# Kernel optimization log

Measured on AMD Instinct MI355X. Metric: run time of the kernel, lower is better.

## Reference

```python
import jax, jax.numpy as jnp
import numpy as np

H = 8
D = 64  # head_dim = node_dim // num_heads = 512 // 8
NODE = 512
EPS = 1e-5


def setup_inputs() -> dict:
    key = jax.random.key(0)
    ks = jax.random.split(key, 8)
    S, IN = 4096, 1024
    return {
        "protT5_emb": jax.random.normal(ks[0], (S, IN), jnp.float32),
        "contact_matrix": jax.random.uniform(ks[1], (S, S), jnp.float32),
        "Wq": jax.random.normal(ks[2], (NODE, IN), jnp.float32) * 0.02,
        "bq": jnp.zeros((NODE,), jnp.float32),
        "Wk": jax.random.normal(ks[3], (NODE, IN), jnp.float32) * 0.02,
        "bk": jnp.zeros((NODE,), jnp.float32),
        "Wv": jax.random.normal(ks[4], (NODE, IN), jnp.float32) * 0.02,
        "bv": jnp.zeros((NODE,), jnp.float32),
        "Wc": jnp.ones((1, H, 1, 1), jnp.float32),
        "Wo": jax.random.normal(ks[5], (NODE, NODE), jnp.float32) * 0.02,
        "bo": jnp.zeros((NODE,), jnp.float32),
        "gamma": jnp.ones((NODE,), jnp.float32),
        "beta": jnp.zeros((NODE,), jnp.float32),
    }


def reference(protT5_emb, contact_matrix, Wq, bq, Wk, bk, Wv, bv, Wc, Wo, bo, gamma, beta):
    S = protT5_emb.shape[0]
    # QKV projections -> [H, S, D]
    Q = (protT5_emb @ Wq.T + bq).reshape(S, H, D).transpose(1, 0, 2)
    K = (protT5_emb @ Wk.T + bk).reshape(S, H, D).transpose(1, 0, 2)
    V = (protT5_emb @ Wv.T + bv).reshape(S, H, D).transpose(1, 0, 2)
    # raw scores [H, S, S]
    attn_raw = jnp.einsum('hsd,htd->hst', Q, K) / jnp.sqrt(jnp.float32(D))
    # multiplicative contact mask, per-head learnable scale
    contact_mask = contact_matrix[None, :, :] * Wc.reshape(H, 1, 1)
    attn_weight = jax.nn.softmax(attn_raw * contact_mask, axis=-1)
    attn_output = jnp.einsum('hst,htd->hsd', attn_weight, V)  # [H, S, D]
    # FAITHFUL to torch: transpose(0,1).view(S,-1) on [1,H,S,D] flattens in
    # (head, seq, dim) order -> scrambled [S, H*D] reshape, not head concat.
    attn_output = attn_output.reshape(S, H * D)
    aug = attn_output @ Wo.T + bo
    x = aug + protT5_emb[:, :NODE]
    mu = jnp.mean(x, axis=-1, keepdims=True)
    var = jnp.mean((x - mu) ** 2, axis=-1, keepdims=True)
    return (x - mu) * jax.lax.rsqrt(var + EPS) * gamma + beta
```

## Files before the change

kernel.cpp:

```cpp
#include <hip/hip_runtime.h>
#include <stdint.h>

#define SEQ 4096
#define INDIM 1024
#define NODEDIM 512
#define NH 8
#define HD 64
#define LSTR 72

typedef __bf16 bf16x8 __attribute__((ext_vector_type(8)));
typedef float f32x4 __attribute__((ext_vector_type(4)));

__device__ __forceinline__ unsigned short f2bf(float f) {
    union { float f; uint32_t u; } v; v.f = f;
    uint32_t u = v.u;
    uint32_t r = (u + 0x7fffu + ((u >> 16) & 1u)) >> 16;
    return (unsigned short)r;
}

__device__ __forceinline__ float fast_exp2(float x) {
    float r;
    asm volatile("v_exp_f32 %0, %1" : "=v"(r) : "v"(x));
    return r;
}

__global__ __launch_bounds__(256) void cvt_all(const float* __restrict__ emb,
                                               const float* __restrict__ Wq,
                                               const float* __restrict__ Wk,
                                               const float* __restrict__ Wv,
                                               const float* __restrict__ Wo,
                                               unsigned short* __restrict__ demb,
                                               unsigned short* __restrict__ dwqkv,
                                               unsigned short* __restrict__ dwo) {
    int b = blockIdx.x;
    const float* src;
    unsigned short* dst;
    int off;
    if (b < 4096)      { src = emb; dst = demb;            off = b; }
    else if (b < 4608) { src = Wq;  dst = dwqkv;           off = b - 4096; }
    else if (b < 5120) { src = Wk;  dst = dwqkv + 524288;  off = b - 4608; }
    else if (b < 5632) { src = Wv;  dst = dwqkv + 1048576; off = b - 5120; }
    else               { src = Wo;  dst = dwo;             off = b - 5632; }
    int i = (off * 256 + threadIdx.x) * 4;
    float4 v = *(const float4*)(src + i);
    ushort4 o;
    o.x = f2bf(v.x); o.y = f2bf(v.y); o.z = f2bf(v.z); o.w = f2bf(v.w);
    *(ushort4*)(dst + i) = o;
}

__global__ __launch_bounds__(256) void qkv_gemm(const unsigned short* __restrict__ A,
                                                const unsigned short* __restrict__ B,
                                                const float* __restrict__ bq,
                                                const float* __restrict__ bk,
                                                const float* __restrict__ bv,
                                                unsigned short* __restrict__ Qo,
                                                unsigned short* __restrict__ Ko,
                                                unsigned short* __restrict__ VTo) {
    __shared__ unsigned short As[128 * 32];
    __shared__ unsigned short Bs[128 * 32];
    __shared__ unsigned short Ts[128 * 40];
    const int tid = threadIdx.x;
    const int lane = tid & 63, wave = tid >> 6;
    const int wm = wave >> 1, wn = wave & 1;
    const int quad = lane >> 4, l16 = lane & 15;
    const int m0 = blockIdx.x * 128;
    const int n0 = blockIdx.y * 128;

    f32x4 acc[4][4] = {};

    for (int k0 = 0; k0 < INDIM; k0 += 32) {
        __syncthreads();
        for (int i = 0; i < 2; ++i) {
            int c = tid + 256 * i;
            int row = c >> 2, qq = c & 3;
            *(bf16x8*)&As[row * 32 + qq * 8] =
                *(const bf16x8*)(A + (size_t)(m0 + row) * INDIM + k0 + qq * 8);
            *(bf16x8*)&Bs[row * 32 + qq * 8] =
                *(const bf16x8*)(B + (size_t)(n0 + row) * INDIM + k0 + qq * 8);
        }
        __syncthreads();
        bf16x8 af[4], bf[4];
        for (int mi = 0; mi < 4; ++mi)
            af[mi] = *(const bf16x8*)&As[(wm * 64 + mi * 16 + l16) * 32 + quad * 8];
        for (int ni = 0; ni < 4; ++ni)
            bf[ni] = *(const bf16x8*)&Bs[(wn * 64 + ni * 16 + l16) * 32 + quad * 8];
        for (int mi = 0; mi < 4; ++mi)
            for (int ni = 0; ni < 4; ++ni)
                acc[mi][ni] = __builtin_amdgcn_mfma_f32_16x16x32_bf16(af[mi], bf[ni], acc[mi][ni], 0, 0, 0);
    }

    if (blockIdx.y < 8) {
        unsigned short* outp = (blockIdx.y < 4) ? Qo : Ko;
        const float* biasp = (blockIdx.y < 4) ? bq : bk;
        for (int mi = 0; mi < 4; ++mi)
            for (int ni = 0; ni < 4; ++ni)
                for (int r = 0; r < 4; ++r) {
                    int s = m0 + wm * 64 + mi * 16 + quad * 4 + r;
                    int n = n0 + wn * 64 + ni * 16 + l16;
                    int h = (n >> 6) & 7;
                    int dd = n & 63;
                    float v = acc[mi][ni][r] + biasp[n & 511];
                    outp[((size_t)h * SEQ + s) * HD + dd] = f2bf(v);
                }
    } else {
        for (int chunk = 0; chunk < 4; ++chunk) {
            const int cwm = chunk >> 1;
            const int milo = (chunk & 1) * 2;
            __syncthreads();
            if (wm == cwm) {
                for (int mi2 = 0; mi2 < 2; ++mi2) {
                    int mi = milo + mi2;
                    for (int ni = 0; ni < 4; ++ni) {
                        int ddf = wn * 64 + ni * 16 + l16;
                        float bias = bv[(n0 + ddf) & 511];
                        for (int r = 0; r < 4; ++r) {
                            int sl = mi2 * 16 + quad * 4 + r;
                            Ts[ddf * 40 + sl] = f2bf(acc[mi][ni][r] + bias);
                        }
                    }
                }
            }
            __syncthreads();
            for (int pass = 0; pass < 2; ++pass) {
                int c = pass * 256 + tid;
                int row = c >> 2, part = c & 3;
                int nfull = n0 + row;
                int h = (nfull >> 6) & 7, dd = nfull & 63;
                *(bf16x8*)(VTo + ((size_t)h * HD + dd) * SEQ + m0 + chunk * 32 + part * 8) =
                    *(const bf16x8*)&Ts[row * 40 + part * 8];
            }
        }
    }
}

__global__ __launch_bounds__(256, 4) void attn_kernel(const unsigned short* __restrict__ Q,
                                                      const unsigned short* __restrict__ K,
                                                      const unsigned short* __restrict__ VT,
                                                      const float* __restrict__ CM,
                                                      const float* __restrict__ Wc,
                                                      float* __restrict__ O0,
                                                      float* __restrict__ O1,
                                                      float* __restrict__ l0,
                                                      float* __restrict__ l1) {
    __shared__ unsigned short QPs[64 * LSTR];
    __shared__ unsigned short Ks[64 * LSTR];
    __shared__ unsigned short Vs[64 * LSTR];
    const int tid = threadIdx.x;
    const int lane = tid & 63, wave = tid >> 6;
    const int quad = lane >> 4, l16 = lane & 15;
    const int h = blockIdx.y;
    const int q0 = blockIdx.x * 64;
    const int split = blockIdx.z;
    float* __restrict__ Op = split ? O1 : O0;
    float* __restrict__ lp = split ? l1 : l0;
    const float wch = Wc[h] * 0.125f * 1.44269504f;

    const int srow0 = tid >> 3, spart = tid & 7;
    const int srow1 = (tid + 256) >> 3;

    {
        bf16x8 v0 = *(const bf16x8*)(Q + ((size_t)h * SEQ + q0 + srow0) * HD + spart * 8);
        bf16x8 v1 = *(const bf16x8*)(Q + ((size_t)h * SEQ + q0 + srow1) * HD + spart * 8);
        for (int j = 0; j < 8; ++j) {
            v0[j] = (__bf16)((float)v0[j] * wch);
            v1[j] = (__bf16)((float)v1[j] * wch);
        }
        *(bf16x8*)&QPs[srow0 * LSTR + spart * 8] = v0;
        *(bf16x8*)&QPs[srow1 * LSTR + spart * 8] = v1;
    }

    const int tbeg = split * (SEQ / 2);
    const int tend = tbeg + SEQ / 2;

    const unsigned short* kp0 = K + ((size_t)h * SEQ + tbeg + srow0) * HD + spart * 8;
    const unsigned short* kp1 = K + ((size_t)h * SEQ + tbeg + srow1) * HD + spart * 8;
    const unsigned short* vp0 = VT + ((size_t)h * HD + srow0) * SEQ + tbeg + spart * 8;
    const unsigned short* vp1 = VT + ((size_t)h * HD + srow1) * SEQ + tbeg + spart * 8;
    bf16x8 kr0 = *(const bf16x8*)kp0;
    bf16x8 kr1 = *(const bf16x8*)kp1;
    bf16x8 vr0 = *(const bf16x8*)vp0;
    bf16x8 vr1 = *(const bf16x8*)vp1;

    __syncthreads();
    bf16x8 a0 = *(const bf16x8*)&QPs[(wave * 16 + l16) * LSTR + quad * 8];
    bf16x8 a1 = *(const bf16x8*)&QPs[(wave * 16 + l16) * LSTR + 32 + quad * 8];

    f32x4 O[4] = {};
    float l_part[4] = {0.f, 0.f, 0.f, 0.f};
    const float* cmbase = CM + (size_t)(q0 + wave * 16 + quad * 4) * SEQ + l16;

    for (int t0 = tbeg; t0 < tend; t0 += 64) {
        float cmv[4][4];
        for (int r = 0; r < 4; ++r)
            for (int nt = 0; nt < 4; ++nt)
                cmv[r][nt] = cmbase[(size_t)r * SEQ + t0 + nt * 16];

        __syncthreads();
        *(bf16x8*)&Ks[srow0 * LSTR + spart * 8] = kr0;
        *(bf16x8*)&Ks[srow1 * LSTR + spart * 8] = kr1;
        *(bf16x8*)&Vs[srow0 * LSTR + spart * 8] = vr0;
        *(bf16x8*)&Vs[srow1 * LSTR + spart * 8] = vr1;
        __syncthreads();

        if (t0 + 64 < tend) {
            kr0 = *(const bf16x8*)(kp0 + (size_t)(t0 + 64 - tbeg) * HD);
            kr1 = *(const bf16x8*)(kp1 + (size_t)(t0 + 64 - tbeg) * HD);
            vr0 = *(const bf16x8*)(vp0 + (t0 + 64 - tbeg));
            vr1 = *(const bf16x8*)(vp1 + (t0 + 64 - tbeg));
        }

        f32x4 sc[4];
        for (int nt = 0; nt < 4; ++nt) {
            bf16x8 b0 = *(const bf16x8*)&Ks[(nt * 16 + l16) * LSTR + quad * 8];
            bf16x8 b1 = *(const bf16x8*)&Ks[(nt * 16 + l16) * LSTR + 32 + quad * 8];
            f32x4 z = {0.f, 0.f, 0.f, 0.f};
            z = __builtin_amdgcn_mfma_f32_16x16x32_bf16(a0, b0, z, 0, 0, 0);
            z = __builtin_amdgcn_mfma_f32_16x16x32_bf16(a1, b1, z, 0, 0, 0);
            sc[nt] = z;
        }

        for (int r = 0; r < 4; ++r) {
            for (int nt = 0; nt < 4; ++nt) {
                float pv = fast_exp2(sc[nt][r] * cmv[r][nt]);
                l_part[r] += pv;
                union { float f; uint32_t u; } pu; pu.f = pv;
                QPs[(wave * 16 + quad * 4 + r) * LSTR + nt * 16 + l16] =
                    (unsigned short)(pu.u >> 16);
            }
        }

        asm volatile("s_waitcnt lgkmcnt(0)" ::: "memory");

        bf16x8 pa0 = *(const bf16x8*)&QPs[(wave * 16 + l16) * LSTR + quad * 8];
        bf16x8 pa1 = *(const bf16x8*)&QPs[(wave * 16 + l16) * LSTR + 32 + quad * 8];
        for (int nt = 0; nt < 4; ++nt) {
            bf16x8 vb0 = *(const bf16x8*)&Vs[(nt * 16 + l16) * LSTR + quad * 8];
            bf16x8 vb1 = *(const bf16x8*)&Vs[(nt * 16 + l16) * LSTR + 32 + quad * 8];
            f32x4 o = O[nt];
            o = __builtin_amdgcn_mfma_f32_16x16x32_bf16(pa0, vb0, o, 0, 0, 0);
            o = __builtin_amdgcn_mfma_f32_16x16x32_bf16(pa1, vb1, o, 0, 0, 0);
            O[nt] = o;
        }
    }

    for (int r = 0; r < 4; ++r) {
        float s = l_part[r];
        for (int off = 1; off < 16; off <<= 1) s += __shfl_xor(s, off);
        l_part[r] = s;
    }
    if (l16 == 0)
        for (int r = 0; r < 4; ++r)
            lp[(size_t)h * SEQ + q0 + wave * 16 + quad * 4 + r] = l_part[r];
    for (int nt = 0; nt < 4; ++nt)
        for (int r = 0; r < 4; ++r) {
            int sg = q0 + wave * 16 + quad * 4 + r;
            Op[((size_t)h * SEQ + sg) * HD + nt * 16 + l16] = O[nt][r];
        }
}

__global__ __launch_bounds__(256) void combine_kernel(const float* __restrict__ O0,
                                                      const float* __restrict__ O1,
                                                      const float* __restrict__ l0,
                                                      const float* __restrict__ l1,
                                                      unsigned short* __restrict__ AO) {
    int idx = blockIdx.x * 256 + threadIdx.x;
    int e = idx * 4;
    int row = e >> 6;
    float4 a = *(const float4*)(O0 + e);
    float4 b = *(const float4*)(O1 + e);
    float linv = 1.f / (l0[row] + l1[row]);
    ushort4 o;
    o.x = f2bf((a.x + b.x) * linv);
    o.y = f2bf((a.y + b.y) * linv);
    o.z = f2bf((a.z + b.z) * linv);
    o.w = f2bf((a.w + b.w) * linv);
    *(ushort4*)(AO + e) = o;
}

__global__ __launch_bounds__(256) void out_gemm(const unsigned short* __restrict__ A,
                                                const unsigned short* __restrict__ B,
                                                const float* __restrict__ bo,
                                                const float* __restrict__ emb,
                                                float* __restrict__ X) {
    __shared__ unsigned short As[64 * 32];
    __shared__ unsigned short Bs[128 * 32];
    const int tid = threadIdx.x;
    const int lane = tid & 63, wave = tid >> 6;
    const int quad = lane >> 4, l16 = lane & 15;
    const int m0 = blockIdx.x * 64;
    const int n0 = blockIdx.y * 128;

    f32x4 acc[8] = {};

    for (int k0 = 0; k0 < NODEDIM; k0 += 32) {
        __syncthreads();
        {
            int row = tid >> 2, qq = tid & 3;
            *(bf16x8*)&As[row * 32 + qq * 8] =
                *(const bf16x8*)(A + (size_t)(m0 + row) * NODEDIM + k0 + qq * 8);
        }
        for (int i = 0; i < 2; ++i) {
            int c = tid + 256 * i;
            int row = c >> 2, qq = c & 3;
            *(bf16x8*)&Bs[row * 32 + qq * 8] =
                *(const bf16x8*)(B + (size_t)(n0 + row) * NODEDIM + k0 + qq * 8);
        }
        __syncthreads();
        bf16x8 af = *(const bf16x8*)&As[(wave * 16 + l16) * 32 + quad * 8];
        for (int ni = 0; ni < 8; ++ni) {
            bf16x8 bf = *(const bf16x8*)&Bs[(ni * 16 + l16) * 32 + quad * 8];
            acc[ni] = __builtin_amdgcn_mfma_f32_16x16x32_bf16(af, bf, acc[ni], 0, 0, 0);
        }
    }

    for (int ni = 0; ni < 8; ++ni)
        for (int r = 0; r < 4; ++r) {
            int s = m0 + wave * 16 + quad * 4 + r;
            int n = n0 + ni * 16 + l16;
            float v = acc[ni][r] + bo[n] + emb[(size_t)s * INDIM + n];
            X[(size_t)s * NODEDIM + n] = v;
        }
}

__global__ __launch_bounds__(256) void ln_kernel(const float* __restrict__ X,
                                                 const float* __restrict__ gamma,
                                                 const float* __restrict__ beta,
                                                 float* __restrict__ out) {
    const int s = blockIdx.x;
    const int n = threadIdx.x * 2;
    float2 v = *(const float2*)&X[(size_t)s * NODEDIM + n];
    float sum = v.x + v.y;
    float sq = v.x * v.x + v.y * v.y;
    for (int off = 32; off > 0; off >>= 1) {
        sum += __shfl_down(sum, off);
        sq += __shfl_down(sq, off);
    }
    __shared__ float ssum[4], ssq[4];
    const int wave = threadIdx.x >> 6, lane = threadIdx.x & 63;
    if (lane == 0) { ssum[wave] = sum; ssq[wave] = sq; }
    __syncthreads();
    float tsum = ssum[0] + ssum[1] + ssum[2] + ssum[3];
    float tsq = ssq[0] + ssq[1] + ssq[2] + ssq[3];
    float mu = tsum * (1.f / 512.f);
    float var = tsq * (1.f / 512.f) - mu * mu;
    float rstd = rsqrtf(var + 1e-5f);
    float2 g = *(const float2*)&gamma[n];
    float2 b = *(const float2*)&beta[n];
    float2 o;
    o.x = (v.x - mu) * rstd * g.x + b.x;
    o.y = (v.y - mu) * rstd * g.y + b.y;
    *(float2*)&out[(size_t)s * NODEDIM + n] = o;
}

extern "C" void kernel_launch(void* const* d_in, const int* in_sizes, int n_in,
                              void* d_out, int out_size, void* d_ws, size_t ws_size,
                              hipStream_t stream) {
    const float* emb = (const float*)d_in[0];
    const float* cm  = (const float*)d_in[1];
    const float* Wq  = (const float*)d_in[2];
    const float* bq  = (const float*)d_in[3];
    const float* Wk  = (const float*)d_in[4];
    const float* bk  = (const float*)d_in[5];
    const float* Wv  = (const float*)d_in[6];
    const float* bv  = (const float*)d_in[7];
    const float* Wc  = (const float*)d_in[8];
    const float* Wo  = (const float*)d_in[9];
    const float* bo  = (const float*)d_in[10];
    const float* gamma = (const float*)d_in[11];
    const float* beta  = (const float*)d_in[12];
    float* out = (float*)d_out;

    unsigned short* ws = (unsigned short*)d_ws;
    unsigned short* emb_bf  = ws;
    unsigned short* wqkv_bf = emb_bf + 4194304;
    unsigned short* wo_bf   = wqkv_bf + 1572864;
    unsigned short* Qb  = wo_bf + 262144;
    unsigned short* Kb  = Qb + 2097152;
    unsigned short* VTb = Kb + 2097152;
    unsigned short* AOb = VTb + 2097152;
    float* X = (float*)(AOb + 2097152);
    float* O0 = (float*)emb_bf;
    float* O1 = X;
    float* l0 = (float*)wqkv_bf;
    float* l1 = l0 + NH * SEQ;

    cvt_all<<<5888, 256, 0, stream>>>(emb, Wq, Wk, Wv, Wo, emb_bf, wqkv_bf, wo_bf);

    qkv_gemm<<<dim3(32, 12), 256, 0, stream>>>(emb_bf, wqkv_bf, bq, bk, bv, Qb, Kb, VTb);
    attn_kernel<<<dim3(64, 8, 2), 256, 0, stream>>>(Qb, Kb, VTb, cm, Wc, O0, O1, l0, l1);
    combine_kernel<<<2048, 256, 0, stream>>>(O0, O1, l0, l1, AOb);
    out_gemm<<<dim3(64, 4), 256, 0, stream>>>(AOb, wo_bf, bo, emb, X);
    ln_kernel<<<4096, 256, 0, stream>>>(X, gamma, beta, out);
}
```

Measured before the change: 260.3 us.

## Use direct global-to-LDS loads in GEMMs and prefetch contact mask one tile ahead

Replaces register-staged global loads into shared memory in the QKV and output GEMMs with global_load_lds builtins, which write straight into LDS and skip the VGPR round trip. In the attention kernel, the contact-matrix values for the next key tile are loaded during the current tile's compute and rotated into place, hiding global latency. Risks: the LDS destination must follow the wave-uniform base plus lane*16 layout that global_load_lds uses, and the extra prefetch registers may cut occupancy.

```diff
diff --git a/kernel.cpp b/kernel.cpp
--- a/kernel.cpp
+++ b/kernel.cpp
@@ -10,6 +10,11 @@
 
 typedef __bf16 bf16x8 __attribute__((ext_vector_type(8)));
 typedef float f32x4 __attribute__((ext_vector_type(4)));
+
+#define GLOAD_LDS(gp, lp) \
+    __builtin_amdgcn_global_load_lds( \
+        (const __attribute__((address_space(1))) void*)(gp), \
+        (__attribute__((address_space(3))) void*)(lp), 16, 0, 0)
 
 __device__ __forceinline__ unsigned short f2bf(float f) {
     union { float f; uint32_t u; } v; v.f = f;
@@ -66,17 +71,16 @@
     const int m0 = blockIdx.x * 128;
     const int n0 = blockIdx.y * 128;
 
+    const int srow = tid >> 2, sqq = tid & 3;
+
     f32x4 acc[4][4] = {};
 
     for (int k0 = 0; k0 < INDIM; k0 += 32) {
         __syncthreads();
         for (int i = 0; i < 2; ++i) {
-            int c = tid + 256 * i;
-            int row = c >> 2, qq = c & 3;
-            *(bf16x8*)&As[row * 32 + qq * 8] =
-                *(const bf16x8*)(A + (size_t)(m0 + row) * INDIM + k0 + qq * 8);
-            *(bf16x8*)&Bs[row * 32 + qq * 8] =
-                *(const bf16x8*)(B + (size_t)(n0 + row) * INDIM + k0 + qq * 8);
+            int row = srow + 64 * i;
+            GLOAD_LDS(A + (size_t)(m0 + row) * INDIM + k0 + sqq * 8, &As[row * 32 + sqq * 8]);
+            GLOAD_LDS(B + (size_t)(n0 + row) * INDIM + k0 + sqq * 8, &Bs[row * 32 + sqq * 8]);
         }
         __syncthreads();
         bf16x8 af[4], bf[4];
@@ -181,20 +185,20 @@
     bf16x8 vr0 = *(const bf16x8*)vp0;
     bf16x8 vr1 = *(const bf16x8*)vp1;
 
+    const float* cmbase = CM + (size_t)(q0 + wave * 16 + quad * 4) * SEQ + l16;
+    float cmv[4][4];
+    for (int r = 0; r < 4; ++r)
+        for (int nt = 0; nt < 4; ++nt)
+            cmv[r][nt] = cmbase[(size_t)r * SEQ + tbeg + nt * 16];
+
     __syncthreads();
     bf16x8 a0 = *(const bf16x8*)&QPs[(wave * 16 + l16) * LSTR + quad * 8];
     bf16x8 a1 = *(const bf16x8*)&QPs[(wave * 16 + l16) * LSTR + 32 + quad * 8];
 
     f32x4 O[4] = {};
     float l_part[4] = {0.f, 0.f, 0.f, 0.f};
-    const float* cmbase = CM + (size_t)(q0 + wave * 16 + quad * 4) * SEQ + l16;
 
     for (int t0 = tbeg; t0 < tend; t0 += 64) {
-        float cmv[4][4];
-        for (int r = 0; r < 4; ++r)
-            for (int nt = 0; nt < 4; ++nt)
-                cmv[r][nt] = cmbase[(size_t)r * SEQ + t0 + nt * 16];
-
         __syncthreads();
         *(bf16x8*)&Ks[srow0 * LSTR + spart * 8] = kr0;
         *(bf16x8*)&Ks[srow1 * LSTR + spart * 8] = kr1;
@@ -202,11 +206,15 @@
         *(bf16x8*)&Vs[srow1 * LSTR + spart * 8] = vr1;
         __syncthreads();
 
+        float cmn[4][4];
         if (t0 + 64 < tend) {
             kr0 = *(const bf16x8*)(kp0 + (size_t)(t0 + 64 - tbeg) * HD);
             kr1 = *(const bf16x8*)(kp1 + (size_t)(t0 + 64 - tbeg) * HD);
             vr0 = *(const bf16x8*)(vp0 + (t0 + 64 - tbeg));
             vr1 = *(const bf16x8*)(vp1 + (t0 + 64 - tbeg));
+            for (int r = 0; r < 4; ++r)
+                for (int nt = 0; nt < 4; ++nt)
+                    cmn[r][nt] = cmbase[(size_t)r * SEQ + t0 + 64 + nt * 16];
         }
 
         f32x4 sc[4];
@@ -228,6 +236,10 @@
                     (unsigned short)(pu.u >> 16);
             }
         }
+
+        for (int r = 0; r < 4; ++r)
+            for (int nt = 0; nt < 4; ++nt)
+                cmv[r][nt] = cmn[r][nt];
 
         asm volatile("s_waitcnt lgkmcnt(0)" ::: "memory");
 
@@ -290,20 +302,16 @@
     const int m0 = blockIdx.x * 64;
     const int n0 = blockIdx.y * 128;
 
+    const int srow = tid >> 2, sqq = tid & 3;
+
     f32x4 acc[8] = {};
 
     for (int k0 = 0; k0 < NODEDIM; k0 += 32) {
         __syncthreads();
-        {
-            int row = tid >> 2, qq = tid & 3;
-            *(bf16x8*)&As[row * 32 + qq * 8] =
-                *(const bf16x8*)(A + (size_t)(m0 + row) * NODEDIM + k0 + qq * 8);
-        }
+        GLOAD_LDS(A + (size_t)(m0 + srow) * NODEDIM + k0 + sqq * 8, &As[srow * 32 + sqq * 8]);
         for (int i = 0; i < 2; ++i) {
-            int c = tid + 256 * i;
-            int row = c >> 2, qq = c & 3;
-            *(bf16x8*)&Bs[row * 32 + qq * 8] =
-                *(const bf16x8*)(B + (size_t)(n0 + row) * NODEDIM + k0 + qq * 8);
+            int row = srow + 64 * i;
+            GLOAD_LDS(B + (size_t)(n0 + row) * NODEDIM + k0 + sqq * 8, &Bs[row * 32 + sqq * 8]);
         }
         __syncthreads();
         bf16x8 af = *(const bf16x8*)&As[(wave * 16 + l16) * 32 + quad * 8];
```

New measurement: 260.6 us. No clear change (+0.1%).
